# Kernel tuning notes

Measured on AMD Instinct MI355X. Metric: run time of the kernel, lower is better.

## Reference

```python
import jax, jax.numpy as jnp
import numpy as np

DIM = 1024
HEADS = 16
DIM_HEAD = 64
INNER = HEADS * DIM_HEAD  # 1024
SCALE = DIM_HEAD ** -0.5


def setup_inputs() -> dict:
    key = jax.random.key(0)
    k1, k2, k3, k4 = jax.random.split(key, 4)
    x = jax.random.normal(k1, (2, 2048, DIM), dtype=jnp.float32)
    # nn.Linear(dim, inner*3, bias=False): weight [3*inner, dim]; store transposed [dim, 3*inner]
    w_qkv = jax.random.normal(k2, (DIM, 3 * INNER), dtype=jnp.float32) * (DIM ** -0.5)
    w_out = jax.random.normal(k3, (INNER, DIM), dtype=jnp.float32) * (INNER ** -0.5)
    b_out = jax.random.normal(k4, (DIM,), dtype=jnp.float32) * 0.02
    return {"x": x, "w_qkv": w_qkv, "w_out": w_out, "b_out": b_out}


def _attention(x, w_qkv, w_out, b_out):
    b, n, _ = x.shape
    qkv = x @ w_qkv  # [b, n, 3*inner]
    q_chunk = qkv[..., :INNER]  # NOTE: source bug — q, k, v all come from chunk 0
    def split_heads(t):
        return t.reshape(b, n, HEADS, DIM_HEAD).transpose(0, 2, 1, 3)  # b h n d
    q = split_heads(q_chunk) * SCALE
    k = split_heads(q_chunk)
    v = split_heads(q_chunk)
    dots = jnp.einsum('bhid,bhjd->bhij', q, k)
    mask_value = -jnp.finfo(dots.dtype).max
    causal_mask = jnp.triu(jnp.ones((n, n), dtype=bool), k=1)
    dots = jnp.where(causal_mask, mask_value, dots)
    attn = jax.nn.softmax(dots, axis=-1)
    out = jnp.einsum('bhij,bhjd->bhid', attn, v)
    out = out.transpose(0, 2, 1, 3).reshape(b, n, INNER)
    return out @ w_out + b_out


def reference(x, w_qkv, w_out, b_out):
    return _attention(x, w_qkv, w_out, b_out)
```

## Files before the change

kernel.cpp:

```cpp
#include <hip/hip_runtime.h>
#include <hip/hip_bf16.h>

typedef __attribute__((ext_vector_type(8))) short short8;
typedef __attribute__((ext_vector_type(4))) short bf16x4;
typedef __attribute__((ext_vector_type(4))) float floatx4;

#define MFMA16(a, b, c) __builtin_amdgcn_mfma_f32_16x16x32_bf16((a), (b), (c), 0, 0, 0)

#if defined(__HIP_DEVICE_COMPILE__)
  #if __has_builtin(__builtin_amdgcn_mfma_f32_16x16x16bf16_1k)
    #define MFMA_PV(a, b, c) __builtin_amdgcn_mfma_f32_16x16x16bf16_1k((a), (b), (c), 0, 0, 0)
  #elif __has_builtin(__builtin_amdgcn_mfma_f32_16x16x16_bf16)
    #define MFMA_PV(a, b, c) __builtin_amdgcn_mfma_f32_16x16x16_bf16((a), (b), (c), 0, 0, 0)
  #else
    #error "no 16x16x16 bf16 MFMA builtin found on device pass"
  #endif
#else
  #define MFMA_PV(a, b, c) (c)
#endif

#define SEQ    2048
#define DIMM   1024
#define HEADS  16
#define DHEAD  64
#define ROWS   4096
#define K1 0.18033688011112043f
#define K2 (-34.62468098133512f)

__global__ void cvt_bf16_kernel(const float* __restrict__ src,
                                __hip_bfloat16* __restrict__ dst) {
    const size_t i = (size_t)(blockIdx.x * 256 + threadIdx.x) * 4;
    floatx4 v = *(const floatx4*)(src + i);
    union { bf16x4 s; __hip_bfloat16 h[4]; } u;
#pragma unroll
    for (int j = 0; j < 4; j++) u.h[j] = __float2bfloat16(v[j]);
    *(bf16x4*)(dst + i) = u.s;
}

__global__ __launch_bounds__(256) void transpose_cvt_kernel(
    const float* __restrict__ W, __hip_bfloat16* __restrict__ WT, int ld) {
    __shared__ __hip_bfloat16 tile[64][72];
    const int tid = threadIdx.x;
    const int r = tid >> 2, c0 = (tid & 3) * 16;
    const int k0 = blockIdx.x * 64;
    const int n0 = blockIdx.y * 64;
    const float* src = W + (size_t)(k0 + r) * ld + n0 + c0;
    union { short8 v; __hip_bfloat16 h[8]; } a0, a1;
#pragma unroll
    for (int j = 0; j < 8; j++) {
        a0.h[j] = __float2bfloat16(src[j]);
        a1.h[j] = __float2bfloat16(src[8 + j]);
    }
    *(short8*)&tile[r][c0]     = a0.v;
    *(short8*)&tile[r][c0 + 8] = a1.v;
    __syncthreads();
    union { short8 v; __hip_bfloat16 h[8]; } u0, u1;
#pragma unroll
    for (int j = 0; j < 8; j++) {
        u0.h[j] = tile[c0 + j][r];
        u1.h[j] = tile[c0 + 8 + j][r];
    }
    __hip_bfloat16* dst = WT + (size_t)(n0 + r) * 1024 + k0 + c0;
    *(short8*)dst       = u0.v;
    *(short8*)(dst + 8) = u1.v;
}

__global__ __launch_bounds__(256) void transpose_t_kernel(
    const __hip_bfloat16* __restrict__ t,
    __hip_bfloat16* __restrict__ Tt) {
    __shared__ __hip_bfloat16 tile[64][72];
    const int tid = threadIdx.x;
    const int r = tid >> 2, c0 = (tid & 3) * 16;
    const int row0 = blockIdx.x * 64;
    const int col0 = blockIdx.y * 64;
    const __hip_bfloat16* src = t + (size_t)(row0 + r) * DIMM + col0 + c0;
    *(short8*)&tile[r][c0]     = *(const short8*)src;
    *(short8*)&tile[r][c0 + 8] = *(const short8*)(src + 8);
    __syncthreads();
    union { short8 v; __hip_bfloat16 h[8]; } u0, u1;
#pragma unroll
    for (int j = 0; j < 8; j++) {
        u0.h[j] = tile[c0 + j][r];
        u1.h[j] = tile[c0 + 8 + j][r];
    }
    __hip_bfloat16* dst = Tt + (size_t)(col0 + r) * ROWS + row0 + c0;
    *(short8*)dst       = u0.v;
    *(short8*)(dst + 8) = u1.v;
}

template <typename CT>
__global__ __launch_bounds__(256) void gemm_bf_kernel(
    const __hip_bfloat16* __restrict__ A,
    const __hip_bfloat16* __restrict__ BT,
    const float* __restrict__ bias,
    CT* __restrict__ C, int M, int N, int K) {
    __shared__ __align__(16) __hip_bfloat16 As[2][64][68];
    __shared__ __align__(16) __hip_bfloat16 Bs[2][64][68];

    const int tid  = threadIdx.x;
    const int lane = tid & 63, wid = tid >> 6;
    const int wm   = wid >> 1, wn = wid & 1;
    const int quad = lane >> 4, l15 = lane & 15;
    const int bm = blockIdx.y * 64, bn = blockIdx.x * 64;

    floatx4 acc[2][2];
#pragma unroll
    for (int r = 0; r < 2; r++)
#pragma unroll
        for (int c = 0; c < 2; c++) acc[r][c] = (floatx4){0.f, 0.f, 0.f, 0.f};

    const int sr = tid >> 2, sc = (tid & 3) * 16;
    short8 ra[2], rb[2];
    auto load_tile = [&](int k0) {
        const __hip_bfloat16* pa = A + (size_t)(bm + sr) * K + k0 + sc;
        ra[0] = *(const short8*)pa; ra[1] = *(const short8*)(pa + 8);
        const __hip_bfloat16* pb = BT + (size_t)(bn + sr) * K + k0 + sc;
        rb[0] = *(const short8*)pb; rb[1] = *(const short8*)(pb + 8);
    };
    auto store_tile = [&](int buf) {
        *(short8*)&As[buf][sr][sc]     = ra[0];
        *(short8*)&As[buf][sr][sc + 8] = ra[1];
        *(short8*)&Bs[buf][sr][sc]     = rb[0];
        *(short8*)&Bs[buf][sr][sc + 8] = rb[1];
    };

    load_tile(0);
    store_tile(0);
    if (K > 64) load_tile(64);
    __syncthreads();

    const int nk = K >> 6;
    for (int kb = 0; kb < nk; ++kb) {
        const int buf = kb & 1;
#pragma unroll
        for (int ks = 0; ks < 2; ks++) {
            short8 af[2], bf[2];
#pragma unroll
            for (int r = 0; r < 2; r++)
                af[r] = *(const short8*)&As[buf][wm * 32 + r * 16 + l15][ks * 32 + quad * 8];
#pragma unroll
            for (int c = 0; c < 2; c++)
                bf[c] = *(const short8*)&Bs[buf][wn * 32 + c * 16 + l15][ks * 32 + quad * 8];
#pragma unroll
            for (int r = 0; r < 2; r++)
#pragma unroll
                for (int c = 0; c < 2; c++)
                    acc[r][c] = MFMA16(af[r], bf[c], acc[r][c]);
        }
        if (kb + 1 < nk) store_tile(buf ^ 1);
        if (kb + 2 < nk) load_tile((kb + 2) << 6);
        __syncthreads();
    }

#pragma unroll
    for (int c = 0; c < 2; c++) {
        const int col = bn + wn * 32 + c * 16 + l15;
        const float bv = bias ? bias[col] : 0.f;
#pragma unroll
        for (int r = 0; r < 2; r++) {
            const int row0 = bm + wm * 32 + r * 16 + quad * 4;
#pragma unroll
            for (int i = 0; i < 4; i++) {
                const float v = acc[r][c][i] + bv;
                if constexpr (__is_same(CT, float))
                    C[(size_t)(row0 + i) * N + col] = v;
                else
                    C[(size_t)(row0 + i) * N + col] = __float2bfloat16(v);
            }
        }
    }
}

template <typename AT, typename CT>
__global__ __launch_bounds__(256) void gemm_fp_kernel(
    const AT* __restrict__ A, const float* __restrict__ B,
    const float* __restrict__ bias, CT* __restrict__ C,
    int M, int N, int K, int ldb) {
    __shared__ __align__(16) __hip_bfloat16 As[2][64][40];
    __shared__ __align__(16) __hip_bfloat16 Bs[2][128][40];
    const int tid = threadIdx.x;
    const int lane = tid & 63, wid = tid >> 6;
    const int wm = wid >> 1, wn = wid & 1;
    const int quad = lane >> 4, l15 = lane & 15;
    const int bm = blockIdx.y * 64, bn = blockIdx.x * 128;
    floatx4 acc[2][4];
#pragma unroll
    for (int r = 0; r < 2; r++)
#pragma unroll
        for (int c = 0; c < 4; c++) acc[r][c] = (floatx4){0.f, 0.f, 0.f, 0.f};
    const int a_lr = tid >> 2, a_lc = (tid & 3) * 8;
    const int b_kr = tid & 31, b_nc = (tid >> 5) * 16;
    floatx4 raf0, raf1; short8 rab; floatx4 rb[4];
    auto load_tile = [&](int k0) {
        const AT* pa = A + (size_t)(bm + a_lr) * K + k0 + a_lc;
        if constexpr (__is_same(AT, float)) {
            raf0 = *(const floatx4*)pa; raf1 = *(const floatx4*)(pa + 4);
        } else { rab = *(const short8*)pa; }
        const float* pb = B + (size_t)(k0 + b_kr) * ldb + bn + b_nc;
#pragma unroll
        for (int q = 0; q < 4; q++) rb[q] = *(const floatx4*)(pb + 4 * q);
    };
    auto store_tile = [&](int buf) {
        if constexpr (__is_same(AT, float)) {
            __align__(16) __hip_bfloat16 hh[8];
#pragma unroll
            for (int j = 0; j < 4; j++) {
                hh[j] = __float2bfloat16(raf0[j]); hh[4 + j] = __float2bfloat16(raf1[j]);
            }
            *(short8*)&As[buf][a_lr][a_lc] = *(short8*)&hh[0];
        } else { *(short8*)&As[buf][a_lr][a_lc] = rab; }
#pragma unroll
        for (int q = 0; q < 4; q++)
#pragma unroll
            for (int j = 0; j < 4; j++)
                Bs[buf][b_nc + 4 * q + j][b_kr] = __float2bfloat16(rb[q][j]);
    };
    load_tile(0); store_tile(0);
    if (K > 32) load_tile(32);
    __syncthreads();
    const int nk = K >> 5;
    for (int kb = 0; kb < nk; ++kb) {
        const int buf = kb & 1;
        short8 af[2], bf[4];
#pragma unroll
        for (int r = 0; r < 2; r++)
            af[r] = *(const short8*)&As[buf][wm * 32 + r * 16 + l15][quad * 8];
#pragma unroll
        for (int c = 0; c < 4; c++)
            bf[c] = *(const short8*)&Bs[buf][wn * 64 + c * 16 + l15][quad * 8];
#pragma unroll
        for (int r = 0; r < 2; r++)
#pragma unroll
            for (int c = 0; c < 4; c++)
                acc[r][c] = MFMA16(af[r], bf[c], acc[r][c]);
        if (kb + 1 < nk) store_tile(buf ^ 1);
        if (kb + 2 < nk) load_tile((kb + 2) << 5);
        __syncthreads();
    }
#pragma unroll
    for (int c = 0; c < 4; c++) {
        const int col = bn + wn * 64 + c * 16 + l15;
        const float bv = bias ? bias[col] : 0.f;
#pragma unroll
        for (int r = 0; r < 2; r++) {
            const int row0 = bm + wm * 32 + r * 16 + quad * 4;
#pragma unroll
            for (int i = 0; i < 4; i++) {
                const float v = acc[r][c][i] + bv;
                if constexpr (__is_same(CT, float)) C[(size_t)(row0 + i) * N + col] = v;
                else C[(size_t)(row0 + i) * N + col] = __float2bfloat16(v);
            }
        }
    }
}

__global__ __launch_bounds__(256) void attn_kernel(
    const __hip_bfloat16* __restrict__ T,
    const __hip_bfloat16* __restrict__ Tt,
    __hip_bfloat16* __restrict__ O) {
    __shared__ __align__(16) __hip_bfloat16 Ks[2][64][68];
    __shared__ __align__(16) __hip_bfloat16 Vt[2][64][68];

    const int tid  = threadIdx.x;
    const int lane = tid & 63, wid = tid >> 6;
    const int quad = lane >> 4, l15 = lane & 15;

    const int bx = blockIdx.x;
    const int half = bx >> 9, idx = bx & 511;
    const int g = idx & 15, h = (idx >> 4) & 15, b = idx >> 8;
    const int qt = half ? g : 31 - g;

    const size_t rowbase = (size_t)b * SEQ;
    const int hoff  = h * DHEAD;
    const int qrow0 = qt * 64;

    short8 qf[2];
    {
        const __hip_bfloat16* qp =
            T + (rowbase + qrow0 + wid * 16 + l15) * DIMM + hoff + quad * 8;
        qf[0] = *(const short8*)qp;
        qf[1] = *(const short8*)(qp + 32);
    }

    float l_lane = 0.f;
    floatx4 accO[4];
#pragma unroll
    for (int dt = 0; dt < 4; dt++) accO[dt] = (floatx4){0.f,0.f,0.f,0.f};

    const int sr = tid >> 2;
    const int sc = (tid & 3) * 16;

    short8 rK0, rK1, rV0, rV1;
    auto load_tile = [&](int kt) {
        const __hip_bfloat16* pK = T + (rowbase + kt * 64 + sr) * DIMM + hoff + sc;
        rK0 = *(const short8*)pK; rK1 = *(const short8*)(pK + 8);
        const __hip_bfloat16* pV =
            Tt + (size_t)(hoff + sr) * ROWS + rowbase + kt * 64 + sc;
        rV0 = *(const short8*)pV; rV1 = *(const short8*)(pV + 8);
    };
    auto store_tile = [&](int buf) {
        *(short8*)&Ks[buf][sr][sc]     = rK0;
        *(short8*)&Ks[buf][sr][sc + 8] = rK1;
        *(short8*)&Vt[buf][sr][sc]     = rV0;
        *(short8*)&Vt[buf][sr][sc + 8] = rV1;
    };

    const int last = qt;
    load_tile(0);
    store_tile(0);
    if (last >= 1) load_tile(1);
    __syncthreads();

    for (int kt = 0; kt <= last; ++kt) {
        const int buf = kt & 1;

        floatx4 s[4];
#pragma unroll
        for (int c = 0; c < 4; c++) {
            s[c] = (floatx4){0.f,0.f,0.f,0.f};
#pragma unroll
            for (int ks = 0; ks < 2; ks++) {
                short8 kfr = *(const short8*)&Ks[buf][c * 16 + l15][ks * 32 + quad * 8];
                s[c] = MFMA16(kfr, qf[ks], s[c]);
            }
        }

        bf16x4 pk[4];
        const bool need_mask = (kt == last);
#pragma unroll
        for (int c = 0; c < 4; c++) {
            union { bf16x4 v; __hip_bfloat16 hh[4]; } u;
            float sum = 0.f;
#pragma unroll
            for (int i = 0; i < 4; i++) {
                float v = exp2f(fmaf(s[c][i], K1, K2));
                if (need_mask) {
                    const int key  = kt * 64 + c * 16 + quad * 4 + i;
                    const int qrow = qrow0 + wid * 16 + l15;
                    if (key > qrow) v = 0.f;
                }
                sum += v;
                u.hh[i] = __float2bfloat16(v);
            }
            l_lane += sum;
            pk[c] = u.v;
        }

#pragma unroll
        for (int c = 0; c < 4; c++)
#pragma unroll
            for (int dt = 0; dt < 4; dt++) {
                bf16x4 vb = *(const bf16x4*)&Vt[buf][dt * 16 + l15][c * 16 + quad * 4];
                accO[dt] = MFMA_PV(pk[c], vb, accO[dt]);
            }

        if (kt < last)      store_tile(buf ^ 1);
        if (kt + 2 <= last) load_tile(kt + 2);
        __syncthreads();
    }

    l_lane += __shfl_xor(l_lane, 16);
    l_lane += __shfl_xor(l_lane, 32);
    float inv[4];
#pragma unroll
    for (int i = 0; i < 4; i++)
        inv[i] = 1.f / __shfl(l_lane, quad * 4 + i, 64);
#pragma unroll
    for (int dt = 0; dt < 4; dt++)
#pragma unroll
        for (int i = 0; i < 4; i++) {
            const size_t row = rowbase + qrow0 + wid * 16 + quad * 4 + i;
            O[row * DIMM + hoff + dt * 16 + l15] =
                __float2bfloat16(accO[dt][i] * inv[i]);
        }
}

extern "C" void kernel_launch(void* const* d_in, const int* in_sizes, int n_in,
                              void* d_out, int out_size, void* d_ws, size_t ws_size,
                              hipStream_t stream) {
    const float* x     = (const float*)d_in[0];
    const float* w_qkv = (const float*)d_in[1];
    const float* w_out = (const float*)d_in[2];
    const float* b_out = (const float*)d_in[3];
    float* out = (float*)d_out;

    __hip_bfloat16* t  = (__hip_bfloat16*)d_out;
    __hip_bfloat16* Tt = (__hip_bfloat16*)((char*)d_out + (8u << 20));
    char* ws = (char*)d_ws;
    __hip_bfloat16* ob = (__hip_bfloat16*)ws;

    if (ws_size >= (size_t)(20u << 20)) {
        __hip_bfloat16* xb  = (__hip_bfloat16*)(ws + (8u  << 20));
        __hip_bfloat16* w1t = (__hip_bfloat16*)(ws + (16u << 20));
        __hip_bfloat16* w2t = (__hip_bfloat16*)(ws + (18u << 20));

        cvt_bf16_kernel<<<4096, 256, 0, stream>>>(x, xb);
        transpose_cvt_kernel<<<dim3(16, 16), 256, 0, stream>>>(w_qkv, w1t, 3 * DIMM);
        transpose_cvt_kernel<<<dim3(16, 16), 256, 0, stream>>>(w_out, w2t, DIMM);

        gemm_bf_kernel<__hip_bfloat16><<<dim3(16, 64), 256, 0, stream>>>(
            xb, w1t, nullptr, t, ROWS, DIMM, DIMM);
        transpose_t_kernel<<<dim3(64, 16), 256, 0, stream>>>(t, Tt);
        attn_kernel<<<dim3(1024), 256, 0, stream>>>(t, Tt, ob);
        gemm_bf_kernel<float><<<dim3(16, 64), 256, 0, stream>>>(
            ob, w2t, b_out, out, ROWS, DIMM, DIMM);
    } else {
        gemm_fp_kernel<float, __hip_bfloat16><<<dim3(8, 64), 256, 0, stream>>>(
            x, w_qkv, nullptr, t, ROWS, DIMM, DIMM, 3 * DIMM);
        transpose_t_kernel<<<dim3(64, 16), 256, 0, stream>>>(t, Tt);
        attn_kernel<<<dim3(1024), 256, 0, stream>>>(t, Tt, ob);
        gemm_fp_kernel<__hip_bfloat16, float><<<dim3(8, 64), 256, 0, stream>>>(
            ob, w_out, b_out, out, ROWS, DIMM, DIMM, DIMM);
    }
}
```

Baseline: 165.5 us.

## Enlarge GEMM and attention tiles, stage GEMM tiles via direct global-to-LDS loads

The bf16 GEMM moves to 128x64 block tiles with four row fragments per wave, and loads tiles straight into LDS with global_load_lds instead of going through registers. Its LDS layout loses the row padding, which may add bank conflicts. The attention kernel now handles 128 query rows per block, two 16-row fragments per wave, so each staged K/V tile is reused twice. It also raises wave priority around the PV MFMAs. Both changes halve the grid sizes, trading fewer, heavier blocks and more registers for less global traffic and fewer synchronisations per FLOP.

```diff
diff --git a/kernel.cpp b/kernel.cpp
--- a/kernel.cpp
+++ b/kernel.cpp
@@ -19,6 +19,12 @@
   #define MFMA_PV(a, b, c) (c)
 #endif
 
+#if defined(__HIP_DEVICE_COMPILE__) && __has_builtin(__builtin_amdgcn_global_load_lds)
+  #define HAVE_GLOAD 1
+#else
+  #define HAVE_GLOAD 0
+#endif
+
 #define SEQ    2048
 #define DIMM   1024
 #define HEADS  16
@@ -26,6 +32,16 @@
 #define ROWS   4096
 #define K1 0.18033688011112043f
 #define K2 (-34.62468098133512f)
+
+__device__ __forceinline__ void gload16(const void* g, void* l) {
+#if HAVE_GLOAD
+    __builtin_amdgcn_global_load_lds(
+        (const __attribute__((address_space(1))) void*)g,
+        (__attribute__((address_space(3))) void*)l, 16, 0, 0);
+#else
+    (void)g; (void)l;
+#endif
+}
 
 __global__ void cvt_bf16_kernel(const float* __restrict__ src,
                                 __hip_bfloat16* __restrict__ dst) {
@@ -94,61 +110,72 @@
     const __hip_bfloat16* __restrict__ BT,
     const float* __restrict__ bias,
     CT* __restrict__ C, int M, int N, int K) {
-    __shared__ __align__(16) __hip_bfloat16 As[2][64][68];
-    __shared__ __align__(16) __hip_bfloat16 Bs[2][64][68];
+    __shared__ __align__(16) __hip_bfloat16 As[2][128][64];
+    __shared__ __align__(16) __hip_bfloat16 Bs[2][64][64];
 
     const int tid  = threadIdx.x;
     const int lane = tid & 63, wid = tid >> 6;
     const int wm   = wid >> 1, wn = wid & 1;
     const int quad = lane >> 4, l15 = lane & 15;
-    const int bm = blockIdx.y * 64, bn = blockIdx.x * 64;
-
-    floatx4 acc[2][2];
-#pragma unroll
-    for (int r = 0; r < 2; r++)
+    const int bm = blockIdx.y * 128, bn = blockIdx.x * 64;
+
+    floatx4 acc[4][2];
+#pragma unroll
+    for (int r = 0; r < 4; r++)
 #pragma unroll
         for (int c = 0; c < 2; c++) acc[r][c] = (floatx4){0.f, 0.f, 0.f, 0.f};
 
-    const int sr = tid >> 2, sc = (tid & 3) * 16;
-    short8 ra[2], rb[2];
-    auto load_tile = [&](int k0) {
-        const __hip_bfloat16* pa = A + (size_t)(bm + sr) * K + k0 + sc;
-        ra[0] = *(const short8*)pa; ra[1] = *(const short8*)(pa + 8);
-        const __hip_bfloat16* pb = BT + (size_t)(bn + sr) * K + k0 + sc;
-        rb[0] = *(const short8*)pb; rb[1] = *(const short8*)(pb + 8);
+    const int to    = tid << 4;
+    const int arow  = to >> 7;
+    const int acol  = (to & 127) >> 1;
+    const int wbase = to & ~1023;
+
+    auto stage = [&](int k0, int buf) {
+#if HAVE_GLOAD
+#pragma unroll
+        for (int j = 0; j < 4; j++)
+            gload16(A + (size_t)(bm + j * 32 + arow) * K + k0 + acol,
+                    (char*)&As[buf][0][0] + j * 4096 + wbase);
+#pragma unroll
+        for (int j = 0; j < 2; j++)
+            gload16(BT + (size_t)(bn + j * 32 + arow) * K + k0 + acol,
+                    (char*)&Bs[buf][0][0] + j * 4096 + wbase);
+#else
+#pragma unroll
+        for (int j = 0; j < 4; j++) {
+            short8 v = *(const short8*)(A + (size_t)(bm + j * 32 + arow) * K + k0 + acol);
+            *(short8*)((char*)&As[buf][0][0] + j * 4096 + to) = v;
+        }
+#pragma unroll
+        for (int j = 0; j < 2; j++) {
+            short8 v = *(const short8*)(BT + (size_t)(bn + j * 32 + arow) * K + k0 + acol);
+            *(short8*)((char*)&Bs[buf][0][0] + j * 4096 + to) = v;
+        }
+#endif
     };
-    auto store_tile = [&](int buf) {
-        *(short8*)&As[buf][sr][sc]     = ra[0];
-        *(short8*)&As[buf][sr][sc + 8] = ra[1];
-        *(short8*)&Bs[buf][sr][sc]     = rb[0];
-        *(short8*)&Bs[buf][sr][sc + 8] = rb[1];
-    };
-
-    load_tile(0);
-    store_tile(0);
-    if (K > 64) load_tile(64);
+
+    stage(0, 0);
     __syncthreads();
 
     const int nk = K >> 6;
     for (int kb = 0; kb < nk; ++kb) {
         const int buf = kb & 1;
+        if (kb + 1 < nk) stage((kb + 1) << 6, buf ^ 1);
 #pragma unroll
         for (int ks = 0; ks < 2; ks++) {
-            short8 af[2], bf[2];
-#pragma unroll
-            for (int r = 0; r < 2; r++)
-                af[r] = *(const short8*)&As[buf][wm * 32 + r * 16 + l15][ks * 32 + quad * 8];
+            short8 af[4], bfr[2];
+#pragma unroll
+            for (int r = 0; r < 4; r++)
+                af[r] = *(const short8*)&As[buf][wm * 64 + r * 16 + l15][ks * 32 + quad * 8];
 #pragma unroll
             for (int c = 0; c < 2; c++)
-                bf[c] = *(const short8*)&Bs[buf][wn * 32 + c * 16 + l15][ks * 32 + quad * 8];
-#pragma unroll
-            for (int r = 0; r < 2; r++)
+                bfr[c] = *(const short8*)&Bs[buf][wn * 32 + c * 16 + l15][ks * 32 + quad * 8];
+#pragma unroll
+            for (int r = 0; r < 4; r++)
 #pragma unroll
                 for (int c = 0; c < 2; c++)
-                    acc[r][c] = MFMA16(af[r], bf[c], acc[r][c]);
-        }
-        if (kb + 1 < nk) store_tile(buf ^ 1);
-        if (kb + 2 < nk) load_tile((kb + 2) << 6);
+                    acc[r][c] = MFMA16(af[r], bfr[c], acc[r][c]);
+        }
         __syncthreads();
     }
 
@@ -157,8 +184,8 @@
         const int col = bn + wn * 32 + c * 16 + l15;
         const float bv = bias ? bias[col] : 0.f;
 #pragma unroll
-        for (int r = 0; r < 2; r++) {
-            const int row0 = bm + wm * 32 + r * 16 + quad * 4;
+        for (int r = 0; r < 4; r++) {
+            const int row0 = bm + wm * 64 + r * 16 + quad * 4;
 #pragma unroll
             for (int i = 0; i < 4; i++) {
                 const float v = acc[r][c][i] + bv;
@@ -266,26 +293,29 @@
     const int quad = lane >> 4, l15 = lane & 15;
 
     const int bx = blockIdx.x;
-    const int half = bx >> 9, idx = bx & 511;
-    const int g = idx & 15, h = (idx >> 4) & 15, b = idx >> 8;
-    const int qt = half ? g : 31 - g;
+    const int half = bx >> 8, idx = bx & 255;
+    const int g = idx & 7, h = (idx >> 3) & 15, b = idx >> 7;
+    const int qt = half ? g : 15 - g;
 
     const size_t rowbase = (size_t)b * SEQ;
     const int hoff  = h * DHEAD;
-    const int qrow0 = qt * 64;
-
-    short8 qf[2];
-    {
+    const int qrow0 = qt * 128;
+
+    short8 qf[2][2];
+#pragma unroll
+    for (int qr = 0; qr < 2; qr++) {
         const __hip_bfloat16* qp =
-            T + (rowbase + qrow0 + wid * 16 + l15) * DIMM + hoff + quad * 8;
-        qf[0] = *(const short8*)qp;
-        qf[1] = *(const short8*)(qp + 32);
-    }
-
-    float l_lane = 0.f;
-    floatx4 accO[4];
-#pragma unroll
-    for (int dt = 0; dt < 4; dt++) accO[dt] = (floatx4){0.f,0.f,0.f,0.f};
+            T + (rowbase + qrow0 + wid * 32 + qr * 16 + l15) * DIMM + hoff + quad * 8;
+        qf[qr][0] = *(const short8*)qp;
+        qf[qr][1] = *(const short8*)(qp + 32);
+    }
+
+    float l_lane[2] = {0.f, 0.f};
+    floatx4 accO[2][4];
+#pragma unroll
+    for (int qr = 0; qr < 2; qr++)
+#pragma unroll
+        for (int dt = 0; dt < 4; dt++) accO[qr][dt] = (floatx4){0.f,0.f,0.f,0.f};
 
     const int sr = tid >> 2;
     const int sc = (tid & 3) * 16;
@@ -305,74 +335,86 @@
         *(short8*)&Vt[buf][sr][sc + 8] = rV1;
     };
 
-    const int last = qt;
+    const int last = 2 * qt + 1;
     load_tile(0);
     store_tile(0);
-    if (last >= 1) load_tile(1);
+    load_tile(1);
     __syncthreads();
 
     for (int kt = 0; kt <= last; ++kt) {
         const int buf = kt & 1;
 
-        floatx4 s[4];
+        bf16x4 pk[2][4];
+        const bool need_mask = (kt >= 2 * qt);
 #pragma unroll
         for (int c = 0; c < 4; c++) {
-            s[c] = (floatx4){0.f,0.f,0.f,0.f};
-#pragma unroll
-            for (int ks = 0; ks < 2; ks++) {
-                short8 kfr = *(const short8*)&Ks[buf][c * 16 + l15][ks * 32 + quad * 8];
-                s[c] = MFMA16(kfr, qf[ks], s[c]);
-            }
-        }
-
-        bf16x4 pk[4];
-        const bool need_mask = (kt == last);
-#pragma unroll
-        for (int c = 0; c < 4; c++) {
-            union { bf16x4 v; __hip_bfloat16 hh[4]; } u;
-            float sum = 0.f;
-#pragma unroll
-            for (int i = 0; i < 4; i++) {
-                float v = exp2f(fmaf(s[c][i], K1, K2));
-                if (need_mask) {
-                    const int key  = kt * 64 + c * 16 + quad * 4 + i;
-                    const int qrow = qrow0 + wid * 16 + l15;
-                    if (key > qrow) v = 0.f;
+            short8 k0 = *(const short8*)&Ks[buf][c * 16 + l15][quad * 8];
+            short8 k1 = *(const short8*)&Ks[buf][c * 16 + l15][32 + quad * 8];
+            floatx4 s[2];
+            s[0] = (floatx4){0.f,0.f,0.f,0.f};
+            s[1] = (floatx4){0.f,0.f,0.f,0.f};
+            s[0] = MFMA16(k0, qf[0][0], s[0]);
+            s[1] = MFMA16(k0, qf[1][0], s[1]);
+            s[0] = MFMA16(k1, qf[0][1], s[0]);
+            s[1] = MFMA16(k1, qf[1][1], s[1]);
+
+#pragma unroll
+            for (int qr = 0; qr < 2; qr++) {
+                union { bf16x4 v; __hip_bfloat16 hh[4]; } u;
+                float sum = 0.f;
+                const int qrow = qrow0 + wid * 32 + qr * 16 + l15;
+#pragma unroll
+                for (int i = 0; i < 4; i++) {
+                    float v = exp2f(fmaf(s[qr][i], K1, K2));
+                    if (need_mask) {
+                        const int key = kt * 64 + c * 16 + quad * 4 + i;
+                        if (key > qrow) v = 0.f;
+                    }
+                    sum += v;
+                    u.hh[i] = __float2bfloat16(v);
                 }
-                sum += v;
-                u.hh[i] = __float2bfloat16(v);
-            }
-            l_lane += sum;
-            pk[c] = u.v;
-        }
-
+                l_lane[qr] += sum;
+                pk[qr][c] = u.v;
+            }
+        }
+
+        __builtin_amdgcn_s_setprio(1);
 #pragma unroll
         for (int c = 0; c < 4; c++)
 #pragma unroll
             for (int dt = 0; dt < 4; dt++) {
                 bf16x4 vb = *(const bf16x4*)&Vt[buf][dt * 16 + l15][c * 16 + quad * 4];
-                accO[dt] = MFMA_PV(pk[c], vb, accO[dt]);
-            }
+                accO[0][dt] = MFMA_PV(pk[0][c], vb, accO[0][dt]);
+                accO[1][dt] = MFMA_PV(pk[1][c], vb, accO[1][dt]);
+            }
+        __builtin_amdgcn_s_setprio(0);
 
         if (kt < last)      store_tile(buf ^ 1);
         if (kt + 2 <= last) load_tile(kt + 2);
         __syncthreads();
     }
 
-    l_lane += __shfl_xor(l_lane, 16);
-    l_lane += __shfl_xor(l_lane, 32);
-    float inv[4];
-#pragma unroll
-    for (int i = 0; i < 4; i++)
-        inv[i] = 1.f / __shfl(l_lane, quad * 4 + i, 64);
-#pragma unroll
-    for (int dt = 0; dt < 4; dt++)
-#pragma unroll
-        for (int i = 0; i < 4; i++) {
-            const size_t row = rowbase + qrow0 + wid * 16 + quad * 4 + i;
-            O[row * DIMM + hoff + dt * 16 + l15] =
-                __float2bfloat16(accO[dt][i] * inv[i]);
-        }
+#pragma unroll
+    for (int qr = 0; qr < 2; qr++) {
+        l_lane[qr] += __shfl_xor(l_lane[qr], 16);
+        l_lane[qr] += __shfl_xor(l_lane[qr], 32);
+    }
+    float inv[2][4];
+#pragma unroll
+    for (int qr = 0; qr < 2; qr++)
+#pragma unroll
+        for (int i = 0; i < 4; i++)
+            inv[qr][i] = 1.f / __shfl(l_lane[qr], quad * 4 + i, 64);
+#pragma unroll
+    for (int qr = 0; qr < 2; qr++)
+#pragma unroll
+        for (int dt = 0; dt < 4; dt++)
+#pragma unroll
+            for (int i = 0; i < 4; i++) {
+                const size_t row = rowbase + qrow0 + wid * 32 + qr * 16 + quad * 4 + i;
+                O[row * DIMM + hoff + dt * 16 + l15] =
+                    __float2bfloat16(accO[qr][dt][i] * inv[qr][i]);
+            }
 }
 
 extern "C" void kernel_launch(void* const* d_in, const int* in_sizes, int n_in,
@@ -398,17 +440,17 @@
         transpose_cvt_kernel<<<dim3(16, 16), 256, 0, stream>>>(w_qkv, w1t, 3 * DIMM);
         transpose_cvt_kernel<<<dim3(16, 16), 256, 0, stream>>>(w_out, w2t, DIMM);
 
-        gemm_bf_kernel<__hip_bfloat16><<<dim3(16, 64), 256, 0, stream>>>(
+        gemm_bf_kernel<__hip_bfloat16><<<dim3(16, 32), 256, 0, stream>>>(
             xb, w1t, nullptr, t, ROWS, DIMM, DIMM);
         transpose_t_kernel<<<dim3(64, 16), 256, 0, stream>>>(t, Tt);
-        attn_kernel<<<dim3(1024), 256, 0, stream>>>(t, Tt, ob);
-        gemm_bf_kernel<float><<<dim3(16, 64), 256, 0, stream>>>(
+        attn_kernel<<<dim3(512), 256, 0, stream>>>(t, Tt, ob);
+        gemm_bf_kernel<float><<<dim3(16, 32), 256, 0, stream>>>(
             ob, w2t, b_out, out, ROWS, DIMM, DIMM);
     } else {
         gemm_fp_kernel<float, __hip_bfloat16><<<dim3(8, 64), 256, 0, stream>>>(
             x, w_qkv, nullptr, t, ROWS, DIMM, DIMM, 3 * DIMM);
         transpose_t_kernel<<<dim3(64, 16), 256, 0, stream>>>(t, Tt);
-        attn_kernel<<<dim3(1024), 256, 0, stream>>>(t, Tt, ob);
+        attn_kernel<<<dim3(512), 256, 0, stream>>>(t, Tt, ob);
         gemm_fp_kernel<__hip_bfloat16, float><<<dim3(8, 64), 256, 0, stream>>>(
             ob, w_out, b_out, out, ROWS, DIMM, DIMM, DIMM);
     }
```

Measured after the change: 176.2 us. 6.5% more time.
